# Optimization experiments

Hardware: AMD Instinct MI355X
Metric: run time of the kernel (lower is better)

Reference implementation:

```python
import jax, jax.numpy as jnp
import numpy as np

B, TX, TY, C, H = 16, 256, 2048, 80, 256
NEG = -1e9


def setup_inputs() -> dict:
    key = jax.random.key(0)
    k = jax.random.split(key, 6)
    en = jax.random.normal(k[0], (B, H, TX), jnp.float32)           # encoder out [B,H,Tx]
    mu = jax.random.normal(k[1], (B, C, TX), jnp.float32)           # MDN means [B,C,Tx]
    log_sigma = 0.1 * jax.random.normal(k[2], (B, C, TX), jnp.float32)
    y = jax.random.normal(k[3], (B, TY, C), jnp.float32)            # mel target [B,Ty,C]
    # lengths near max so y_len >= x_len (monotonic path exists)
    x_lengths = TX - jax.random.randint(k[4], (B,), 0, 64, dtype=jnp.int32)
    y_lengths = TY - jax.random.randint(k[5], (B,), 0, 512, dtype=jnp.int32)
    return {"en": en, "mu": mu, "log_sigma": log_sigma, "y": y,
            "x_lengths": x_lengths, "y_lengths": y_lengths}


def compute_log_probs(mu, log_sigma, y):
    """logp[b,x,t] = -0.5*mean_c[(y[b,t,c]-mu[b,x,c])^2/sigma^2] - 0.5*mean_c[log_sigma].
    Expanded as y^2 - 2*y*mu + mu^2 to avoid materializing [B,Tx,Ty,C]."""
    mu_t = jnp.swapaxes(mu, 1, 2)          # [B,Tx,C]
    ls_t = jnp.swapaxes(log_sigma, 1, 2)   # [B,Tx,C]
    inv_var = jnp.exp(-2.0 * ls_t)         # 1/sigma^2
    t1 = jnp.einsum('byc,bxc->bxy', y * y, inv_var)
    t2 = jnp.einsum('byc,bxc->bxy', y, mu_t * inv_var)
    t3 = jnp.sum(mu_t * mu_t * inv_var, axis=-1)[..., None]
    expo = -0.5 * (t1 - 2.0 * t2 + t3) / C
    return expo - 0.5 * jnp.mean(ls_t, axis=-1, keepdims=True)  # [B,Tx,Ty]


def _mas_single(logp, x_len, y_len):
    """Viterbi monotonic alignment search for one batch item. logp: [Tx,Ty]."""
    tx, ty = logp.shape
    ii = jnp.arange(tx)
    row_ok = ii < x_len

    def fwd(v_prev, col):
        shifted = jnp.concatenate([jnp.full((1,), NEG, v_prev.dtype), v_prev[:-1]])
        diag = shifted > v_prev                      # came from i-1
        v = jnp.maximum(v_prev, shifted) + col
        v = jnp.where(row_ok, v, NEG)
        return v, diag

    v0 = jnp.where(ii == 0, 0.0, NEG).astype(logp.dtype)
    _, diag = jax.lax.scan(fwd, v0, jnp.swapaxes(logp, 0, 1))  # diag: [Ty,Tx] bool

    def bwd(idx, inp):
        d_j, j = inp
        active = j < y_len
        row = jnp.where(active, (ii == idx).astype(logp.dtype), 0.0)
        new_idx = jnp.where(active, idx - d_j[idx].astype(idx.dtype), idx)
        new_idx = jnp.maximum(new_idx, 0)
        return new_idx, row

    idx0 = (x_len - 1).astype(jnp.int32)
    _, rows = jax.lax.scan(bwd, idx0, (diag, jnp.arange(ty)), reverse=True)
    return jnp.swapaxes(rows, 0, 1)  # path [Tx,Ty]


def maximum_path(logp, x_lengths, y_lengths):
    return jax.vmap(_mas_single)(logp, x_lengths, y_lengths)


def generate_path(dr, x_mask, y_mask):
    """Durations [B,Tx] -> hard alignment [B,Tx,Ty]."""
    cum = jnp.cumsum(dr, axis=-1)                                  # [B,Tx]
    j = jnp.arange(y_mask.shape[-1], dtype=dr.dtype)
    m = (j[None, None, :] < cum[:, :, None]).astype(dr.dtype)      # [B,Tx,Ty]
    path = m - jnp.concatenate([jnp.zeros_like(m[:, :1]), m[:, :-1]], axis=1)
    return path * (x_mask[:, :, None] * y_mask[:, None, :])


def reference(en, mu, log_sigma, y, x_lengths, y_lengths):
    x_mask = (jnp.arange(TX)[None, :] < x_lengths[:, None]).astype(en.dtype)
    y_mask = (jnp.arange(TY)[None, :] < y_lengths[:, None]).astype(en.dtype)
    logp = compute_log_probs(mu, log_sigma, y)                     # [B,Tx,Ty]
    attn_mas = jax.lax.stop_gradient(maximum_path(logp, x_lengths, y_lengths))
    dr_mas = jnp.sum(attn_mas, axis=-1)                            # [B,Tx]
    attn = generate_path(dr_mas, x_mask, y_mask)                   # [B,Tx,Ty]
    o_en_ex = jnp.einsum('bxy,bcx->bcy', attn, en)                 # [B,H,Ty]
    return (o_en_ex, attn, dr_mas, logp)
```

## Files before the change

### kernel.cpp

```cpp
#include <hip/hip_runtime.h>
#include <hip/hip_bf16.h>
#include <cstdint>
#include <cstddef>

#define B_ 16
#define TX_ 256
#define TY_ 2048
#define C_ 80
#define H_ 256
#define NEG_ -1e9f
#define NEG_I (int)0xCE6E6B28

#define BT_STEP(JB)                                                           \
    {                                                                         \
        unsigned bit = ((unsigned)(W >> (((ii & 7) << 3)                      \
                                         | (7 - (JB)))) & 1u)                 \
                     & (unsigned)(ii > 0);                                    \
        ii -= (int)bit;                                                       \
        W = (bit && ((ii & 7) == 7)) ? Wl : W;                                \
    }

__global__ __launch_bounds__(256) void logp_kernel(
    const float* __restrict__ mu, const float* __restrict__ ls,
    const float* __restrict__ y, float* __restrict__ logp_out,
    float* __restrict__ logp_t)
{
    __shared__ float2 coef[16 * 80];
    __shared__ float  aux[16 * 80];
    __shared__ float  Kx[16];
    __shared__ float  yt[16 * 1028];

    const int tid = threadIdx.x;
    const int t0 = blockIdx.x * 1024;
    const int x0 = blockIdx.y * 16;
    const int b  = blockIdx.z;

    for (int i = tid; i < 16 * 80; i += 256) {
        int c = i >> 4, x = i & 15;
        float m = mu[(size_t)(b * C_ + c) * TX_ + x0 + x];
        float l = ls[(size_t)(b * C_ + c) * TX_ + x0 + x];
        float w = __expf(-2.f * l);
        coef[x * 80 + c] = make_float2(w, -2.f * m * w);
        aux[x * 80 + c]  = fmaf(m * m, w, l);
    }
    __syncthreads();
    if (tid < 16) {
        float s = 0.f;
        for (int c = 0; c < C_; ++c) s += aux[tid * 80 + c];
        Kx[tid] = -0.5f * s / (float)C_;
    }

    float acc[16][4];
#pragma unroll
    for (int x = 0; x < 16; ++x)
#pragma unroll
        for (int r = 0; r < 4; ++r) acc[x][r] = 0.f;

    const float4* y4 = (const float4*)y;
    for (int c0 = 0; c0 < C_; c0 += 16) {
        __syncthreads();
        for (int it = 0; it < 16; ++it) {
            int f = tid + it * 256;
            int t = f >> 2, k = f & 3;
            float4 v = y4[(size_t)(b * TY_ + t0 + t) * 20 + (c0 >> 2) + k];
            yt[(4 * k + 0) * 1028 + t] = v.x;
            yt[(4 * k + 1) * 1028 + t] = v.y;
            yt[(4 * k + 2) * 1028 + t] = v.z;
            yt[(4 * k + 3) * 1028 + t] = v.w;
        }
        __syncthreads();
        for (int cl = 0; cl < 16; ++cl) {
            const float4 yv = *reinterpret_cast<const float4*>(&yt[cl * 1028 + 4 * tid]);
            float4 y2 = make_float4(yv.x * yv.x, yv.y * yv.y, yv.z * yv.z, yv.w * yv.w);
#pragma unroll
            for (int x = 0; x < 16; ++x) {
                float2 f2 = coef[x * 80 + c0 + cl];
                acc[x][0] = fmaf(y2.x, f2.x, fmaf(yv.x, f2.y, acc[x][0]));
                acc[x][1] = fmaf(y2.y, f2.x, fmaf(yv.y, f2.y, acc[x][1]));
                acc[x][2] = fmaf(y2.z, f2.x, fmaf(yv.z, f2.y, acc[x][2]));
                acc[x][3] = fmaf(y2.w, f2.x, fmaf(yv.w, f2.y, acc[x][3]));
            }
        }
    }

#pragma unroll
    for (int x = 0; x < 16; ++x) {
        float kx = Kx[x];
#pragma unroll
        for (int r = 0; r < 4; ++r) acc[x][r] = fmaf(acc[x][r], -0.5f / (float)C_, kx);
        float4 out = make_float4(acc[x][0], acc[x][1], acc[x][2], acc[x][3]);
        *reinterpret_cast<float4*>(
            &logp_out[(size_t)(b * TX_ + x0 + x) * TY_ + t0 + 4 * tid]) = out;
    }
#pragma unroll
    for (int r = 0; r < 4; ++r) {
#pragma unroll
        for (int q = 0; q < 4; ++q) {
            float4 out = make_float4(acc[4 * q + 0][r], acc[4 * q + 1][r],
                                     acc[4 * q + 2][r], acc[4 * q + 3][r]);
            *reinterpret_cast<float4*>(
                &logp_t[(size_t)(b * TY_ + t0 + 4 * tid + r) * TX_ + x0 + 4 * q]) = out;
        }
    }
}

#define PROQ(A, Bq, Cq, Dq) \
    "global_load_dwordx4 " A ", %[vo], %[sb]\n\t" \
    "global_load_dwordx4 " Bq ", %[vo], %[sb] offset:0x400\n\t" \
    "global_load_dwordx4 " Cq ", %[vo], %[sb] offset:0x800\n\t" \
    "global_load_dwordx4 " Dq ", %[vo], %[sb] offset:0xC00\n\t" \
    "v_add_u32 %[vo], 0x1000, %[vo]\n\t"

#define ADDVO "v_add_u32 %[vo], 0x1000, %[vo]\n\t"

#define COLN(RQ, R0, R1, R2, R3, SHU, SHD, OFF) \
    "v_cmp_gt_f32 vcc, " SHU ", %[v0]\n\t" \
    "v_cmp_gt_f32 s[20:21], %[v0], %[v1]\n\t" \
    "v_cmp_gt_f32 s[22:23], %[v1], %[v2]\n\t" \
    "v_cmp_gt_f32 s[24:25], %[v2], %[v3]\n\t" \
    "v_max_f32 %[v3], %[v2], %[v3]\n\t" \
    "v_max_f32 %[v2], %[v1], %[v2]\n\t" \
    "v_add_f32 %[v3], " R3 ", %[v3]\n\t" \
    "v_max_f32 %[v1], %[v0], %[v1]\n\t" \
    "v_max_f32 %[v0], " SHU ", %[v0]\n\t" \
    "v_mov_b32_dpp " SHD ", %[v3] wave_shr:1 row_mask:0xf bank_mask:0xf\n\t" \
    "v_add_f32 %[v2], " R2 ", %[v2]\n\t" \
    "v_add_f32 %[v1], " R1 ", %[v1]\n\t" \
    "v_add_f32 %[v0], " R0 ", %[v0]\n\t" \
    "v_addc_co_u32 %[a0], vcc, %[a0], %[a0], vcc\n\t" \
    "v_addc_co_u32 %[a1], s[20:21], %[a1], %[a1], s[20:21]\n\t" \
    "v_addc_co_u32 %[a2], s[22:23], %[a2], %[a2], s[22:23]\n\t" \
    "v_addc_co_u32 %[a3], s[24:25], %[a3], %[a3], s[24:25]\n\t" \
    "global_load_dwordx4 " RQ ", %[vo], %[sb] offset:" OFF "\n\t"

#define STOREBLK(OFFD) \
    "v_lshl_or_b32 v29, %[a1], 8, %[a0]\n\t" \
    "v_lshl_or_b32 v29, %[a2], 16, v29\n\t" \
    "v_lshl_or_b32 v29, %[a3], 24, v29\n\t" \
    "global_store_dword %[df], v29, %[db] offset:" OFFD "\n\t" \
    "v_mov_b32 %[a0], 0\n\t" \
    "v_mov_b32 %[a1], 0\n\t" \
    "v_mov_b32 %[a2], 0\n\t" \
    "v_mov_b32 %[a3], 0\n\t"

#define WAITG "s_waitcnt vmcnt(24)\n\t"

__global__ __launch_bounds__(64, 1) void mas_fwd_kernel(
    const float* __restrict__ logp_t, unsigned int* __restrict__ diag_g)
{
    const int lane = threadIdx.x;
    const int b = blockIdx.x;

    uint64_t sb = (uint64_t)(logp_t + (size_t)b * TY_ * TX_);
    uint64_t db = (uint64_t)(diag_g + (size_t)b * (TY_ / 8) * 64);
    unsigned vo = (unsigned)(lane * 16);
    unsigned df = (unsigned)(lane * 4);

    float v0 = (lane == 0) ? 0.f : NEG_, v1 = NEG_, v2 = NEG_, v3 = NEG_;
    unsigned a0 = 0, a1 = 0, a2 = 0, a3 = 0;

    asm volatile(
        "v_mov_b32 v28, 0xce6e6b28\n\t"
        "v_mov_b32 v30, 0xce6e6b28\n\t"
        PROQ("v[32:35]",   "v[36:39]",   "v[40:43]",   "v[44:47]")
        PROQ("v[48:51]",   "v[52:55]",   "v[56:59]",   "v[60:63]")
        PROQ("v[64:67]",   "v[68:71]",   "v[72:75]",   "v[76:79]")
        PROQ("v[80:83]",   "v[84:87]",   "v[88:91]",   "v[92:95]")
        PROQ("v[96:99]",   "v[100:103]", "v[104:107]", "v[108:111]")
        PROQ("v[112:115]", "v[116:119]", "v[120:123]", "v[124:127]")
        PROQ("v[128:131]", "v[132:135]", "v[136:139]", "v[140:143]")
        PROQ("v[144:147]", "v[148:151]", "v[152:155]", "v[156:159]")
        "s_mov_b32 s26, 64\n\t"
        "Lmas_%=:\n\t"
        WAITG
        COLN("v[32:35]", "v32", "v33", "v34", "v35", "v28", "v30", "0")
        COLN("v[36:39]", "v36", "v37", "v38", "v39", "v30", "v28", "0x400")
        COLN("v[40:43]", "v40", "v41", "v42", "v43", "v28", "v30", "0x800")
        COLN("v[44:47]", "v44", "v45", "v46", "v47", "v30", "v28", "0xC00")
        ADDVO
        COLN("v[48:51]", "v48", "v49", "v50", "v51", "v28", "v30", "0")
        COLN("v[52:55]", "v52", "v53", "v54", "v55", "v30", "v28", "0x400")
        COLN("v[56:59]", "v56", "v57", "v58", "v59", "v28", "v30", "0x800")
        COLN("v[60:63]", "v60", "v61", "v62", "v63", "v30", "v28", "0xC00")
        ADDVO
        STOREBLK("0")
        WAITG
        COLN("v[64:67]", "v64", "v65", "v66", "v67", "v28", "v30", "0")
        COLN("v[68:71]", "v68", "v69", "v70", "v71", "v30", "v28", "0x400")
        COLN("v[72:75]", "v72", "v73", "v74", "v75", "v28", "v30", "0x800")
        COLN("v[76:79]", "v76", "v77", "v78", "v79", "v30", "v28", "0xC00")
        ADDVO
        COLN("v[80:83]", "v80", "v81", "v82", "v83", "v28", "v30", "0")
        COLN("v[84:87]", "v84", "v85", "v86", "v87", "v30", "v28", "0x400")
        COLN("v[88:91]", "v88", "v89", "v90", "v91", "v28", "v30", "0x800")
        COLN("v[92:95]", "v92", "v93", "v94", "v95", "v30", "v28", "0xC00")
        ADDVO
        STOREBLK("0x100")
        WAITG
        COLN("v[96:99]",   "v96",  "v97",  "v98",  "v99",  "v28", "v30", "0")
        COLN("v[100:103]", "v100", "v101", "v102", "v103", "v30", "v28", "0x400")
        COLN("v[104:107]", "v104", "v105", "v106", "v107", "v28", "v30", "0x800")
        COLN("v[108:111]", "v108", "v109", "v110", "v111", "v30", "v28", "0xC00")
        ADDVO
        COLN("v[112:115]", "v112", "v113", "v114", "v115", "v28", "v30", "0")
        COLN("v[116:119]", "v116", "v117", "v118", "v119", "v30", "v28", "0x400")
        COLN("v[120:123]", "v120", "v121", "v122", "v123", "v28", "v30", "0x800")
        COLN("v[124:127]", "v124", "v125", "v126", "v127", "v30", "v28", "0xC00")
        ADDVO
        STOREBLK("0x200")
        WAITG
        COLN("v[128:131]", "v128", "v129", "v130", "v131", "v28", "v30", "0")
        COLN("v[132:135]", "v132", "v133", "v134", "v135", "v30", "v28", "0x400")
        COLN("v[136:139]", "v136", "v137", "v138", "v139", "v28", "v30", "0x800")
        COLN("v[140:143]", "v140", "v141", "v142", "v143", "v30", "v28", "0xC00")
        ADDVO
        COLN("v[144:147]", "v144", "v145", "v146", "v147", "v28", "v30", "0")
        COLN("v[148:151]", "v148", "v149", "v150", "v151", "v30", "v28", "0x400")
        COLN("v[152:155]", "v152", "v153", "v154", "v155", "v28", "v30", "0x800")
        COLN("v[156:159]", "v156", "v157", "v158", "v159", "v30", "v28", "0xC00")
        ADDVO
        STOREBLK("0x300")
        "v_add_u32 %[df], 0x400, %[df]\n\t"
        "s_sub_u32 s26, s26, 1\n\t"
        "s_cmp_lg_u32 s26, 0\n\t"
        "s_cbranch_scc1 Lmas_%=\n\t"
        : [v0]"+v"(v0), [v1]"+v"(v1), [v2]"+v"(v2), [v3]"+v"(v3),
          [a0]"+v"(a0), [a1]"+v"(a1), [a2]"+v"(a2), [a3]"+v"(a3),
          [vo]"+v"(vo), [df]"+v"(df)
        : [sb]"s"(sb), [db]"s"(db)
        : "vcc", "scc", "memory",
          "s20","s21","s22","s23","s24","s25","s26",
          "v28","v29","v30",
          "v32","v33","v34","v35","v36","v37","v38","v39",
          "v40","v41","v42","v43","v44","v45","v46","v47",
          "v48","v49","v50","v51","v52","v53","v54","v55",
          "v56","v57","v58","v59","v60","v61","v62","v63",
          "v64","v65","v66","v67","v68","v69","v70","v71",
          "v72","v73","v74","v75","v76","v77","v78","v79",
          "v80","v81","v82","v83","v84","v85","v86","v87",
          "v88","v89","v90","v91","v92","v93","v94","v95",
          "v96","v97","v98","v99","v100","v101","v102","v103",
          "v104","v105","v106","v107","v108","v109","v110","v111",
          "v112","v113","v114","v115","v116","v117","v118","v119",
          "v120","v121","v122","v123","v124","v125","v126","v127",
          "v128","v129","v130","v131","v132","v133","v134","v135",
          "v136","v137","v138","v139","v140","v141","v142","v143",
          "v144","v145","v146","v147","v148","v149","v150","v151",
          "v152","v153","v154","v155","v156","v157","v158","v159");
}

__global__ __launch_bounds__(256) void mas_tab_kernel(
    const unsigned int* __restrict__ diag_g, unsigned char* __restrict__ E_g)
{
    const int t  = threadIdx.x;
    const int cg = blockIdx.x;
    const int b  = blockIdx.y;
    const unsigned int* dg = diag_g + (size_t)b * (TY_ / 8) * 64;
    unsigned char* Eb = E_g + (size_t)b * (TY_ / 8) * 256;
    const int p = t >> 3;

    for (int k = 0; k < 16; ++k) {
        const int c = cg * 16 + k;
        unsigned long long W  = *(const unsigned long long*)&dg[c * 64 + 2 * p];
        unsigned long long Wl = p > 0
            ? *(const unsigned long long*)&dg[c * 64 + 2 * (p - 1)] : 0ULL;
        int ii = t;
#pragma unroll
        for (int jb = 7; jb >= 0; --jb) BT_STEP(jb)
        Eb[c * 256 + t] = (unsigned char)ii;
    }
}

__global__ __launch_bounds__(256) void mas_bt_kernel(
    const unsigned int* __restrict__ diag_g, const unsigned char* __restrict__ E_g,
    const int* __restrict__ xlen, const int* __restrict__ ylen,
    float* __restrict__ dr_out, int* __restrict__ idx_out)
{
    __shared__ unsigned char E[256 * 256];
    __shared__ unsigned char entry_s[256];
    __shared__ int rows_l[TY_];
    __shared__ int cnt_l[TX_];
    const int tid = threadIdx.x;
    const int b = blockIdx.x;
    const int x_len = xlen[b];
    const int y_len = ylen[b];

    cnt_l[tid] = 0;

    const uint4* srcE = (const uint4*)(E_g + (size_t)b * (TY_ / 8) * 256);
    uint4* dstE = (uint4*)E;
#pragma unroll
    for (int it = 0; it < 16; ++it)
        dstE[tid + it * 256] = srcE[tid + it * 256];
    __syncthreads();

    const unsigned int* dg = diag_g + (size_t)b * (TY_ / 8) * 64;
    int* ib = idx_out + (size_t)b * TY_;
    const int jc = (y_len - 1) >> 3;

    if (tid == 0) {
        int ii = x_len - 1;
        int p = ii >> 3;
        unsigned long long W  = *(const unsigned long long*)&dg[jc * 64 + 2 * p];
        unsigned long long Wl = p > 0
            ? *(const unsigned long long*)&dg[jc * 64 + 2 * (p - 1)] : 0ULL;
        for (int jb = (y_len - 1) & 7; jb >= 0; --jb) {
            int j = 8 * jc + jb;
            ib[j] = ii; rows_l[j] = ii;
            BT_STEP(jb)
        }
        int cur = ii;
        for (int c = jc - 1; c >= 0; --c) {
            entry_s[c] = (unsigned char)cur;
            cur = E[c * 256 + cur];
        }
    }
    __syncthreads();

    if (tid < jc) {
        const int c = tid;
        int ii = entry_s[c];
        int p = ii >> 3;
        unsigned long long W  = *(const unsigned long long*)&dg[c * 64 + 2 * p];
        unsigned long long Wl = p > 0
            ? *(const unsigned long long*)&dg[c * 64 + 2 * (p - 1)] : 0ULL;
        int r[8];
#pragma unroll
        for (int jb = 7; jb >= 0; --jb) {
            r[jb] = ii;
            BT_STEP(jb)
        }
        *reinterpret_cast<int4*>(&ib[8 * c])     = make_int4(r[0], r[1], r[2], r[3]);
        *reinterpret_cast<int4*>(&ib[8 * c + 4]) = make_int4(r[4], r[5], r[6], r[7]);
        *reinterpret_cast<int4*>(&rows_l[8 * c])     = make_int4(r[0], r[1], r[2], r[3]);
        *reinterpret_cast<int4*>(&rows_l[8 * c + 4]) = make_int4(r[4], r[5], r[6], r[7]);
    }
    __syncthreads();

    for (int t = tid; t < TY_; t += 256)
        if (t < y_len) atomicAdd(&cnt_l[rows_l[t]], 1);
    __syncthreads();
    dr_out[(size_t)b * TX_ + tid] = (float)cnt_l[tid];
}

__global__ __launch_bounds__(256) void emit_kernel(
    const float* __restrict__ en, const int* __restrict__ ylen,
    const int* __restrict__ idx_in, float* __restrict__ o_en,
    float* __restrict__ attn)
{
    const int tid = threadIdx.x;
    const int b = blockIdx.x;
    const int r = blockIdx.y;
    const int y_len = ylen[b];
    const int* ib = idx_in + (size_t)b * TY_;

    if (r < 256) {
        const int x = r;
        float* out = attn + ((size_t)b * TX_ + x) * TY_;
        for (int t = tid; t < TY_; t += 256) {
            int ii = ib[t];
            out[t] = (t < y_len && ii == x) ? 1.f : 0.f;
        }
    } else {
        const int h = r - 256;
        __shared__ float enr[256];
        enr[tid] = en[((size_t)b * H_ + h) * TX_ + tid];
        __syncthreads();
        float* out = o_en + ((size_t)b * H_ + h) * TY_;
        for (int t = tid; t < TY_; t += 256) {
            int ii = ib[t];
            bool a = (t < y_len);
            int is = a ? ii : 0;
            out[t] = a ? enr[is] : 0.f;
        }
    }
}

__global__ __launch_bounds__(256) void emit_sparse_kernel(
    const float* __restrict__ en, const int* __restrict__ ylen,
    const int* __restrict__ idx_in, float* __restrict__ o_en,
    float* __restrict__ attn)
{
    const int tid = threadIdx.x;
    const int b = blockIdx.x;
    const int r = blockIdx.y;
    const int y_len = ylen[b];
    const int* ib = idx_in + (size_t)b * TY_;

    if (r == 256) {
        float* ab = attn + (size_t)b * TX_ * TY_;
        for (int t = tid; t < TY_; t += 256)
            if (t < y_len) ab[(size_t)ib[t] * TY_ + t] = 1.f;
    } else {
        const int h = r;
        __shared__ float enr[256];
        enr[tid] = en[((size_t)b * H_ + h) * TX_ + tid];
        __syncthreads();
        float* out = o_en + ((size_t)b * H_ + h) * TY_;
        for (int t = tid; t < TY_; t += 256) {
            int ii = ib[t];
            bool a = (t < y_len);
            int is = a ? ii : 0;
            out[t] = a ? enr[is] : 0.f;
        }
    }
}

extern "C" void kernel_launch(void* const* d_in, const int* in_sizes, int n_in,
                              void* d_out, int out_size, void* d_ws, size_t ws_size,
                              hipStream_t stream)
{
    const float* en = (const float*)d_in[0];
    const float* mu = (const float*)d_in[1];
    const float* ls = (const float*)d_in[2];
    const float* y  = (const float*)d_in[3];
    const int* xl   = (const int*)d_in[4];
    const int* yl   = (const int*)d_in[5];

    float* o_en = (float*)d_out;
    float* attn = o_en + (size_t)B_ * TX_ * TY_;
    float* dr   = attn + (size_t)B_ * TX_ * TY_;
    float* logp = dr + (size_t)B_ * TX_;

    const size_t logp_t_bytes = (size_t)B_ * TX_ * TY_ * 4;
    const size_t E_bytes      = (size_t)B_ * (TY_ / 8) * 256;
    const size_t idx_bytes    = (size_t)B_ * TY_ * 4;

    unsigned int* diag_g = (unsigned int*)o_en;

    float* logp_t;
    unsigned char* E_g;
    int* idxArr;
    bool sparse;
    if (ws_size >= logp_t_bytes + E_bytes + idx_bytes) {
        logp_t = (float*)d_ws;
        E_g    = (unsigned char*)d_ws + logp_t_bytes;
        idxArr = (int*)((char*)d_ws + logp_t_bytes + E_bytes);
        sparse = true;
    } else {
        logp_t = attn;
        E_g    = (unsigned char*)attn;
        idxArr = (int*)d_ws;
        sparse = false;
    }

    dim3 g1(2, 16, 16);
    logp_kernel<<<g1, 256, 0, stream>>>(mu, ls, y, logp, logp_t);

    mas_fwd_kernel<<<dim3(16), dim3(64), 0, stream>>>(logp_t, diag_g);
    mas_tab_kernel<<<dim3(16, 16), dim3(256), 0, stream>>>(diag_g, E_g);
    mas_bt_kernel<<<dim3(16), dim3(256), 0, stream>>>(diag_g, E_g, xl, yl, dr, idxArr);

    if (sparse) {
        dim3 g3(16, 257);
        emit_sparse_kernel<<<g3, 256, 0, stream>>>(en, yl, idxArr, o_en, attn);
    } else {
        dim3 g3(16, 512);
        emit_kernel<<<g3, 256, 0, stream>>>(en, yl, idxArr, o_en, attn);
    }
}
```

Measured before the change: 282.4 us.

## Add two-level jump table to shorten serial MAS backtrack entry-point chain

The table kernel now also composes each group of 16 per-column-chunk backtrack maps into one 256-entry map per group, stored in a scratch region inside the output buffer. The backtrack kernel's single thread then walks at most about 16 composed maps plus 16 chunk maps instead of up to 255 chained lookups. Threads then expand the per-chunk entry points for each group in parallel. This shortens the serial dependency chain, at the cost of extra shared memory, an extra sync, and a small amount of extra global traffic.

```diff
diff --git a/kernel.cpp b/kernel.cpp
--- a/kernel.cpp
+++ b/kernel.cpp
@@ -250,8 +250,10 @@
 }
 
 __global__ __launch_bounds__(256) void mas_tab_kernel(
-    const unsigned int* __restrict__ diag_g, unsigned char* __restrict__ E_g)
-{
+    const unsigned int* __restrict__ diag_g, unsigned char* __restrict__ E_g,
+    unsigned char* __restrict__ E2_g)
+{
+    __shared__ unsigned char El[16][256];
     const int t  = threadIdx.x;
     const int cg = blockIdx.x;
     const int b  = blockIdx.y;
@@ -268,16 +270,25 @@
 #pragma unroll
         for (int jb = 7; jb >= 0; --jb) BT_STEP(jb)
         Eb[c * 256 + t] = (unsigned char)ii;
-    }
+        El[k][t] = (unsigned char)ii;
+    }
+    __syncthreads();
+    int ii = t;
+#pragma unroll
+    for (int k = 15; k >= 0; --k) ii = El[k][ii];
+    E2_g[((size_t)b * 16 + cg) * 256 + t] = (unsigned char)ii;
 }
 
 __global__ __launch_bounds__(256) void mas_bt_kernel(
     const unsigned int* __restrict__ diag_g, const unsigned char* __restrict__ E_g,
+    const unsigned char* __restrict__ E2_g,
     const int* __restrict__ xlen, const int* __restrict__ ylen,
     float* __restrict__ dr_out, int* __restrict__ idx_out)
 {
     __shared__ unsigned char E[256 * 256];
+    __shared__ unsigned char E2l[16 * 256];
     __shared__ unsigned char entry_s[256];
+    __shared__ unsigned char cg_entry[16];
     __shared__ int rows_l[TY_];
     __shared__ int cnt_l[TX_];
     const int tid = threadIdx.x;
@@ -292,11 +303,14 @@
 #pragma unroll
     for (int it = 0; it < 16; ++it)
         dstE[tid + it * 256] = srcE[tid + it * 256];
+    const uint4* srcE2 = (const uint4*)(E2_g + (size_t)b * 16 * 256);
+    ((uint4*)E2l)[tid] = srcE2[tid];
     __syncthreads();
 
     const unsigned int* dg = diag_g + (size_t)b * (TY_ / 8) * 64;
     int* ib = idx_out + (size_t)b * TY_;
     const int jc = (y_len - 1) >> 3;
+    const int cg0 = jc >> 4;
 
     if (tid == 0) {
         int ii = x_len - 1;
@@ -310,7 +324,21 @@
             BT_STEP(jb)
         }
         int cur = ii;
-        for (int c = jc - 1; c >= 0; --c) {
+        for (int c = jc - 1; c >= cg0 * 16; --c) {
+            entry_s[c] = (unsigned char)cur;
+            cur = E[c * 256 + cur];
+        }
+        for (int cg = cg0 - 1; cg >= 0; --cg) {
+            cg_entry[cg] = (unsigned char)cur;
+            cur = E2l[cg * 256 + cur];
+        }
+    }
+    __syncthreads();
+
+    if (tid < cg0) {
+        int cur = cg_entry[tid];
+        for (int k = 15; k >= 0; --k) {
+            int c = tid * 16 + k;
             entry_s[c] = (unsigned char)cur;
             cur = E[c * 256 + cur];
         }
@@ -427,6 +455,7 @@
     const size_t idx_bytes    = (size_t)B_ * TY_ * 4;
 
     unsigned int* diag_g = (unsigned int*)o_en;
+    unsigned char* E2_g = (unsigned char*)o_en + (1u << 21);
 
     float* logp_t;
     unsigned char* E_g;
@@ -448,8 +477,9 @@
     logp_kernel<<<g1, 256, 0, stream>>>(mu, ls, y, logp, logp_t);
 
     mas_fwd_kernel<<<dim3(16), dim3(64), 0, stream>>>(logp_t, diag_g);
-    mas_tab_kernel<<<dim3(16, 16), dim3(256), 0, stream>>>(diag_g, E_g);
-    mas_bt_kernel<<<dim3(16), dim3(256), 0, stream>>>(diag_g, E_g, xl, yl, dr, idxArr);
+    mas_tab_kernel<<<dim3(16, 16), dim3(256), 0, stream>>>(diag_g, E_g, E2_g);
+    mas_bt_kernel<<<dim3(16), dim3(256), 0, stream>>>(diag_g, E_g, E2_g,
+                                                      xl, yl, dr, idxArr);
 
     if (sparse) {
         dim3 g3(16, 257);
```

Result: faster. 276.6 us, median of 2 (-2.0%).
